# Kernel optimization log

Hardware: AMD Instinct MI355X
Metric: run time of the kernel (lower is better)

The kernel has to match this reference:

```python
import jax, jax.numpy as jnp
import numpy as np

SEQ = 8192
DIM = 1024

def setup_inputs() -> dict:
    key = jax.random.key(0)
    kx, kq, kk, kv1, kv2 = jax.random.split(key, 5)
    std = 0.01  # flax nn.initializers.normal() default stddev=1e-2
    return {
        "x": jax.random.normal(kx, (SEQ, DIM), dtype=jnp.float32),
        "wq": jax.random.normal(kq, (DIM, DIM), dtype=jnp.float32) * std,
        "wk": jax.random.normal(kk, (DIM, DIM), dtype=jnp.float32) * std,
        "wv1": jax.random.normal(kv1, (DIM, DIM), dtype=jnp.float32) * std,
        "wv2": jax.random.normal(kv2, (DIM, DIM), dtype=jnp.float32) * std,
    }

def reference(x, wq, wk, wv1, wv2):
    # x: [S, D]; single-head causal self-attention with SiLU-gated output proj
    q = x @ wq              # [S, D]
    k = x @ wk              # [S, D]
    v = x @ wv1             # [S, D]
    dim_head = q.shape[-1]
    dots = (q @ k.T) * (dim_head ** -0.5)          # [S, S]
    s = x.shape[-2]
    mask = jnp.tril(jnp.ones((s, s), dtype=bool))
    dots = jnp.where(mask, dots, -1e9)
    attn = jax.nn.softmax(dots, axis=-1)            # [S, S]
    hidden = attn @ v                               # [S, D]
    return jax.nn.silu(hidden) @ wv2                # [S, D]
```

## Files before the change

kernel.cpp:

```cpp
#include <hip/hip_runtime.h>
#include <hip/hip_bf16.h>
#include <cstdint>
#include <cstddef>

constexpr int SEQ = 8192;
constexpr int DIM = 1024;

typedef __attribute__((ext_vector_type(8))) short short8;
typedef __attribute__((ext_vector_type(4))) float f32x4;
typedef __attribute__((ext_vector_type(4))) unsigned short us4;

#define MFMA_BF16 __builtin_amdgcn_mfma_f32_16x16x32_bf16

static __device__ __forceinline__ unsigned short f2bf(float f) {
    uint32_t u = __builtin_bit_cast(uint32_t, f);
    u += 0x7FFFu + ((u >> 16) & 1u);
    return (unsigned short)(u >> 16);
}
static __device__ __forceinline__ float bf2f(unsigned short h) {
    uint32_t u = ((uint32_t)h) << 16;
    return __builtin_bit_cast(float, u);
}
static __device__ __forceinline__ int r64(int x) {
    return ((x + 32) >> 6) << 6;
}

#define GLOAD16(gp, lp) __builtin_amdgcn_global_load_lds(                      \
    (const __attribute__((address_space(1))) void*)(gp),                       \
    (__attribute__((address_space(3))) void*)(lp), 16, 0, 0)

template<int OM, bool CAUSAL, bool KCAP, bool SPLITK>
__global__ __launch_bounds__(256, 4)
void gemm_bt(const unsigned short* __restrict__ A,
             const unsigned short* __restrict__ Bt,
             void* __restrict__ Cp,
             int M, int N, int K, float scale, int rowBase, int NS,
             float* __restrict__ Sp)
{
    constexpr int BM = 128, BK = 64, BN = 128;
    constexpr int NF = BN / 32;
    __shared__ __align__(16) unsigned short As[BM * BK];
    __shared__ __align__(16) unsigned short Bs[BN * BK];

    const int t = threadIdx.x;
    const int lane = t & 63, w = t >> 6;
    const int wr = w >> 1, wc = w & 1;
    const int ln15 = lane & 15, hi = lane >> 4;

    const int gx = gridDim.x, gy = gridDim.y;
    const int nwg = gx * gy * gridDim.z;
    const int orig = blockIdx.y + gy * (blockIdx.x + gx * blockIdx.z);
    const int q = nwg >> 3, r8 = nwg & 7;
    const int xcd = orig & 7, idx = orig >> 3;
    const int wg = (xcd < r8 ? xcd * (q + 1)
                             : r8 * (q + 1) + (xcd - r8) * q) + idx;
    const int byi = wg % gy, tmpw = wg / gy;
    const int bxi = tmpw % gx, bzi = tmpw / gx;

    const int bm = byi * BM, bn = bxi * BN;

    if (CAUSAL && bn > rowBase + bm + (BM - 1)) return;
    int Keff = K;
    if (KCAP) { int kc = rowBase + bm + BM; Keff = kc < K ? kc : K; }
    int kbeg = 0, kend = Keff;
    if (SPLITK) {
        kbeg = r64(bzi * Keff / NS);
        int ke = r64((bzi + 1) * Keff / NS);
        kend = ke < Keff ? ke : Keff;
        if (kbeg >= kend) return;
    }

    f32x4 acc[4][NF] = {};

    for (int k0 = kbeg; k0 < kend; k0 += BK) {
        #pragma unroll
        for (int i = 0; i < 4; ++i) {
            int c = t + 256 * i;
            int r = c >> 3, qq = (c & 7) ^ (r & 7);
            GLOAD16(A + (size_t)(bm + r) * K + k0 + qq * 8, As + c * 8);
        }
        #pragma unroll
        for (int i = 0; i < 4; ++i) {
            int c = t + 256 * i;
            int r = c >> 3, qq = (c & 7) ^ (r & 7);
            GLOAD16(Bt + (size_t)(bn + r) * K + k0 + qq * 8, Bs + c * 8);
        }
        __syncthreads();

        #pragma unroll
        for (int kk = 0; kk < 2; ++kk) {
            short8 a[4], b[NF];
            #pragma unroll
            for (int m = 0; m < 4; ++m) {
                int r = wr * 64 + m * 16 + ln15;
                int s = (kk * 4 + hi) ^ (r & 7);
                a[m] = *(const short8*)(As + r * 64 + s * 8);
            }
            #pragma unroll
            for (int n = 0; n < NF; ++n) {
                int r = wc * 64 + n * 16 + ln15;
                int s = (kk * 4 + hi) ^ (r & 7);
                b[n] = *(const short8*)(Bs + r * 64 + s * 8);
            }
            __builtin_amdgcn_s_setprio(1);
            #pragma unroll
            for (int m = 0; m < 4; ++m)
                #pragma unroll
                for (int n = 0; n < NF; ++n)
                    acc[m][n] = MFMA_BF16(a[m], b[n], acc[m][n], 0, 0, 0);
            __builtin_amdgcn_s_setprio(0);
        }
        __syncthreads();
    }

    if (OM == 5) {
        float psum[4][4];
        #pragma unroll
        for (int m = 0; m < 4; ++m)
            #pragma unroll
            for (int j = 0; j < 4; ++j) {
                int row = bm + wr * 64 + m * 16 + hi * 4 + j;
                int grow = rowBase + row;
                float s = 0.f;
                #pragma unroll
                for (int n = 0; n < NF; ++n) {
                    int col = bn + wc * 64 + n * 16 + ln15;
                    float p = (col <= grow)
                        ? __expf(acc[m][n][j] * scale) : 0.f;
                    ((unsigned short*)Cp)[(size_t)row * N + col] = f2bf(p);
                    s += p;
                }
                psum[m][j] = s;
            }
        #pragma unroll
        for (int off = 1; off < 16; off <<= 1)
            #pragma unroll
            for (int m = 0; m < 4; ++m)
                #pragma unroll
                for (int j = 0; j < 4; ++j)
                    psum[m][j] += __shfl_xor(psum[m][j], off, 64);
        if (ln15 == 0) {
            const int ci = bxi * 2 + wc;
            #pragma unroll
            for (int m = 0; m < 4; ++m)
                #pragma unroll
                for (int j = 0; j < 4; ++j)
                    Sp[(size_t)(bm + wr * 64 + m * 16 + hi * 4 + j) * 128 + ci]
                        = psum[m][j];
        }
        return;
    }
    #pragma unroll
    for (int m = 0; m < 4; ++m)
        #pragma unroll
        for (int n = 0; n < NF; ++n)
            #pragma unroll
            for (int j = 0; j < 4; ++j) {
                int row = bm + wr * 64 + m * 16 + hi * 4 + j;
                int col = bn + wc * 64 + n * 16 + ln15;
                float v = acc[m][n][j] * scale;
                if (OM == 0)
                    ((unsigned short*)Cp)[(size_t)row * N + col] = f2bf(v);
                else if (OM == 2)
                    ((float*)Cp)[(size_t)row * N + col] = v;
                else if (OM == 3)
                    ((unsigned short*)Cp + (size_t)bzi * M * N)
                        [(size_t)row * N + col] = f2bf(v);
                else {
                    unsigned short* qb = (unsigned short*)Cp;
                    if (col < DIM)
                        qb[(size_t)row * DIM + col] = f2bf(v);
                    else if (col < 2 * DIM)
                        (qb + (size_t)SEQ * DIM)
                            [(size_t)row * DIM + (col - DIM)] = f2bf(v);
                    else
                        (qb + (size_t)2 * SEQ * DIM)
                            [(size_t)(col - 2 * DIM) * SEQ + row] = f2bf(v);
                }
            }
}

__global__ __launch_bounds__(256)
void reduce_silu(const unsigned short* __restrict__ part,
                 const float* __restrict__ Sp,
                 unsigned short* __restrict__ out, int ns, int rowBase, int bsz)
{
    __shared__ float red[4];
    const int t = threadIdx.x, lane = t & 63, w = t >> 6;
    const size_t idx = ((size_t)blockIdx.x * 256 + t) * 8;
    const int r = (int)(idx >> 10);
    int keb = rowBase + ((r >> 7) << 7) + 128;
    if (keb > SEQ) keb = SEQ;

    {
        const int rloc = blockIdx.x * 2 + (t >> 7);
        const int seg = t & 127;
        const int nct = 2 * (((rowBase + rloc) >> 7) + 1);
        float val = (seg < nct) ? Sp[(size_t)rloc * 128 + seg] : 0.f;
        #pragma unroll
        for (int off = 1; off < 64; off <<= 1)
            val += __shfl_xor(val, off, 64);
        if (lane == 0) red[w] = val;
    }
    __syncthreads();
    const float inv = 1.0f /
        ((t < 128) ? (red[0] + red[1]) : (red[2] + red[3]));

    float s[8] = {};
    for (int z = 0; z < ns; ++z) {
        int b0 = r64(z * keb / ns);
        int b1 = r64((z + 1) * keb / ns);
        if (b1 > keb) b1 = keb;
        if (b1 > b0) {
            short8 p = *(const short8*)(part + (size_t)z * bsz * DIM + idx);
            #pragma unroll
            for (int j = 0; j < 8; ++j) s[j] += bf2f((unsigned short)p[j]);
        }
    }
    short8 o;
    #pragma unroll
    for (int j = 0; j < 8; ++j) {
        float v = s[j] * inv;
        o[j] = (short)f2bf(v / (1.0f + __expf(-v)));
    }
    *(short8*)(out + idx) = o;
}

__global__ __launch_bounds__(256)
void cvt_bf16(const float* __restrict__ X, unsigned short* __restrict__ Y)
{
    int i = (blockIdx.x * 256 + threadIdx.x) * 8;
    f32x4 v0 = *(const f32x4*)(X + i);
    f32x4 v1 = *(const f32x4*)(X + i + 4);
    short8 o = { (short)f2bf(v0[0]), (short)f2bf(v0[1]),
                 (short)f2bf(v0[2]), (short)f2bf(v0[3]),
                 (short)f2bf(v1[0]), (short)f2bf(v1[1]),
                 (short)f2bf(v1[2]), (short)f2bf(v1[3]) };
    *(short8*)(Y + i) = o;
}

static __device__ __forceinline__ void twT_body(
    const float* __restrict__ W, unsigned short* __restrict__ WT)
{
    __shared__ float tile[64][65];
    const int bx = blockIdx.x * 64, by = blockIdx.y * 64;
    const int t = threadIdx.x, rr = t >> 4, c4 = (t & 15) * 4;
    #pragma unroll
    for (int i = 0; i < 4; ++i) {
        int r = rr + i * 16;
        f32x4 v = *(const f32x4*)(W + (size_t)(by + r) * DIM + bx + c4);
        tile[r][c4 + 0] = v[0]; tile[r][c4 + 1] = v[1];
        tile[r][c4 + 2] = v[2]; tile[r][c4 + 3] = v[3];
    }
    __syncthreads();
    #pragma unroll
    for (int i = 0; i < 4; ++i) {
        int r = rr + i * 16;
        us4 o = { f2bf(tile[c4 + 0][r]), f2bf(tile[c4 + 1][r]),
                  f2bf(tile[c4 + 2][r]), f2bf(tile[c4 + 3][r]) };
        *(us4*)(WT + (size_t)(bx + r) * DIM + by + c4) = o;
    }
}

__global__ __launch_bounds__(256)
void twT(const float* __restrict__ W, unsigned short* __restrict__ WT)
{
    twT_body(W, WT);
}

__global__ __launch_bounds__(256)
void twT3(const float* __restrict__ W0, const float* __restrict__ W1,
          const float* __restrict__ W2, unsigned short* __restrict__ WT)
{
    const float* W = (blockIdx.z == 0) ? W0 : (blockIdx.z == 1) ? W1 : W2;
    twT_body(W, WT + (size_t)blockIdx.z * DIM * DIM);
}

extern "C" void kernel_launch(void* const* d_in, const int* in_sizes, int n_in,
                              void* d_out, int out_size, void* d_ws, size_t ws_size,
                              hipStream_t stream)
{
    const float* x   = (const float*)d_in[0];
    const float* wq  = (const float*)d_in[1];
    const float* wk  = (const float*)d_in[2];
    const float* wv1 = (const float*)d_in[3];
    const float* wv2 = (const float*)d_in[4];

    const size_t E = (size_t)SEQ * DIM;
    unsigned short* qbuf  = (unsigned short*)d_ws;
    unsigned short* kbuf  = qbuf + E;
    unsigned short* vtbuf = kbuf + E;
    unsigned short* wsfree = vtbuf + E;
    const size_t avail = ws_size - 3 * E * sizeof(unsigned short);

    unsigned short* xb    = (unsigned short*)d_out;
    unsigned short* wqkv  = xb + E;

    int bandsz;
    unsigned short *Sband, *part;
    float* Sp;
    int nsplit = 4;
    const size_t need4096 = (size_t)4096 * SEQ * 2
                          + (size_t)4 * 4096 * DIM * 2
                          + (size_t)4096 * 128 * 4;
    if (avail >= need4096) {
        bandsz = 4096;
        Sband  = wsfree;
        part   = Sband + (size_t)4096 * SEQ;
        Sp     = (float*)(part + (size_t)4 * 4096 * DIM);
    } else {
        bandsz = 2048;
        Sband  = (unsigned short*)d_out;
        part   = wsfree;
        Sp     = (float*)(part + (size_t)4 * 2048 * DIM);
        if (avail < (size_t)4 * 2048 * DIM * 2 + (size_t)2048 * 128 * 4)
            nsplit = 1;
    }

    cvt_bf16<<<SEQ * DIM / 2048, 256, 0, stream>>>(x, xb);
    twT3<<<dim3(16, 16, 3), 256, 0, stream>>>(wq, wk, wv1, wqkv);

    gemm_bt<4,false,false,false><<<dim3(3 * DIM / 128, SEQ / 128), 256, 0, stream>>>(
        xb, wqkv, qbuf, SEQ, 3 * DIM, DIM, 1.0f, 0, 0, nullptr);

    for (int rb = 0; rb < SEQ; rb += bandsz) {
        const int ncol = (rb + bandsz) / 128;
        dim3 gq(ncol, bandsz / 128);
        gemm_bt<5,true,false,false><<<gq, 256, 0, stream>>>(
            qbuf + (size_t)rb * DIM, kbuf, Sband, bandsz, SEQ, DIM,
            0.03125f, rb, 0, Sp);
        if (rb + bandsz == SEQ)
            twT<<<dim3(16, 16), 256, 0, stream>>>(wv2, kbuf);
        dim3 gpv(DIM / 128, bandsz / 128, nsplit);
        gemm_bt<3,false,true,true><<<gpv, 256, 0, stream>>>(
            Sband, vtbuf, part, bandsz, DIM, SEQ, 1.0f, rb, nsplit, nullptr);
        reduce_silu<<<bandsz * DIM / 2048, 256, 0, stream>>>(
            part, Sp, qbuf + (size_t)rb * DIM, nsplit, rb, bandsz);
    }

    gemm_bt<2,false,false,false><<<dim3(DIM / 128, SEQ / 128), 256, 0, stream>>>(
        qbuf, kbuf, d_out, SEQ, DIM, DIM, 1.0f, 0, 0, nullptr);
}
```

Measured before the change: 347.1 us.

## Use dedicated 256x256-tile 512-thread kernel for fused QKV projection GEMM

Replaces the generic 128x128 gemm_bt launch for the QKV projection with a specialized kernel using 256x256 output tiles, 8 waves, double-buffered swizzled LDS staging and an XCD-aware workgroup remap. Larger tiles raise arithmetic intensity and cut global reloads of A and B, and the remap aims to improve L2 locality per XCD. The cost is 128KB of LDS per block, which limits occupancy to one block per CU, and a grid of only 384 blocks, which may leave the tail underfilled.

```diff
diff --git a/kernel.cpp b/kernel.cpp
--- a/kernel.cpp
+++ b/kernel.cpp
@@ -180,6 +180,109 @@
             }
 }
 
+__global__ __launch_bounds__(512, 1)
+void qkv_gemm8(const unsigned short* __restrict__ A,
+               const unsigned short* __restrict__ Bt,
+               unsigned short* __restrict__ qb, int K)
+{
+    __shared__ __align__(16) unsigned short As[2][256 * 64];
+    __shared__ __align__(16) unsigned short Bs[2][256 * 64];
+
+    const int t = threadIdx.x;
+    const int lane = t & 63, w = t >> 6;
+    const int wr = w >> 2, wc = w & 3;
+    const int ln15 = lane & 15, hi = lane >> 4;
+
+    const int gx = gridDim.x, gy = gridDim.y;
+    const int nwg = gx * gy;
+    const int orig = blockIdx.y + gy * blockIdx.x;
+    const int q = nwg >> 3, r8 = nwg & 7;
+    const int xcd = orig & 7, idx = orig >> 3;
+    const int wg = (xcd < r8 ? xcd * (q + 1)
+                             : r8 * (q + 1) + (xcd - r8) * q) + idx;
+    const int byi = wg % gy, bxi = wg / gy;
+    const int bm = byi * 256, bn = bxi * 256;
+
+#define STAGE8(buf, k0) do {                                                   \
+        _Pragma("unroll")                                                      \
+        for (int i = 0; i < 4; ++i) {                                          \
+            int c = t + 512 * i;                                               \
+            int r = c >> 3, qq = (c & 7) ^ (r & 7);                            \
+            GLOAD16(A + (size_t)(bm + r) * K + (k0) + qq * 8,                  \
+                    &As[buf][c * 8]);                                          \
+        }                                                                      \
+        _Pragma("unroll")                                                      \
+        for (int i = 0; i < 4; ++i) {                                          \
+            int c = t + 512 * i;                                               \
+            int r = c >> 3, qq = (c & 7) ^ (r & 7);                            \
+            GLOAD16(Bt + (size_t)(bn + r) * K + (k0) + qq * 8,                 \
+                    &Bs[buf][c * 8]);                                          \
+        }                                                                      \
+    } while (0)
+
+    f32x4 acc[8][4] = {};
+
+    STAGE8(0, 0);
+    int cur = 0;
+    for (int k0 = 0; k0 < K; k0 += 64) {
+        if (k0 + 64 < K) {
+            STAGE8(cur ^ 1, k0 + 64);
+            asm volatile("s_waitcnt vmcnt(8)" ::: "memory");
+        } else {
+            asm volatile("s_waitcnt vmcnt(0)" ::: "memory");
+        }
+        __builtin_amdgcn_s_barrier();
+        asm volatile("" ::: "memory");
+
+        #pragma unroll
+        for (int kk = 0; kk < 2; ++kk) {
+            short8 a[8], b[4];
+            #pragma unroll
+            for (int m = 0; m < 8; ++m) {
+                int r = wr * 128 + m * 16 + ln15;
+                int s = (kk * 4 + hi) ^ (r & 7);
+                a[m] = *(const short8*)(&As[cur][r * 64 + s * 8]);
+            }
+            #pragma unroll
+            for (int n = 0; n < 4; ++n) {
+                int r = wc * 64 + n * 16 + ln15;
+                int s = (kk * 4 + hi) ^ (r & 7);
+                b[n] = *(const short8*)(&Bs[cur][r * 64 + s * 8]);
+            }
+            __builtin_amdgcn_s_setprio(1);
+            #pragma unroll
+            for (int m = 0; m < 8; ++m)
+                #pragma unroll
+                for (int n = 0; n < 4; ++n)
+                    acc[m][n] = MFMA_BF16(a[m], b[n], acc[m][n], 0, 0, 0);
+            __builtin_amdgcn_s_setprio(0);
+        }
+        asm volatile("" ::: "memory");
+        __builtin_amdgcn_s_barrier();
+        cur ^= 1;
+    }
+#undef STAGE8
+
+    #pragma unroll
+    for (int m = 0; m < 8; ++m)
+        #pragma unroll
+        for (int n = 0; n < 4; ++n)
+            #pragma unroll
+            for (int j = 0; j < 4; ++j) {
+                int row = bm + wr * 128 + m * 16 + hi * 4 + j;
+                int col = bn + wc * 64 + n * 16 + ln15;
+                unsigned short v = f2bf(acc[m][n][j]);
+                if (col < DIM)
+                    qb[(size_t)row * DIM + col] = v;
+                else if (col < 2 * DIM)
+                    (qb + (size_t)SEQ * DIM)
+                        [(size_t)row * DIM + (col - DIM)] = v;
+                else
+                    (qb + (size_t)2 * SEQ * DIM)
+                        [(size_t)(col - 2 * DIM) * SEQ + row] = v;
+            }
+}
+
 __global__ __launch_bounds__(256)
 void reduce_silu(const unsigned short* __restrict__ part,
                  const float* __restrict__ Sp,
@@ -320,8 +423,8 @@
     cvt_bf16<<<SEQ * DIM / 2048, 256, 0, stream>>>(x, xb);
     twT3<<<dim3(16, 16, 3), 256, 0, stream>>>(wq, wk, wv1, wqkv);
 
-    gemm_bt<4,false,false,false><<<dim3(3 * DIM / 128, SEQ / 128), 256, 0, stream>>>(
-        xb, wqkv, qbuf, SEQ, 3 * DIM, DIM, 1.0f, 0, 0, nullptr);
+    qkv_gemm8<<<dim3(3 * DIM / 256, SEQ / 256), 512, 0, stream>>>(
+        xb, wqkv, qbuf, DIM);
 
     for (int rb = 0; rb < SEQ; rb += bandsz) {
         const int ncol = (rb + bandsz) / 128;
```

New measurement: 367.8 us. 6.0% more time.
